# Kernel optimization log

Hardware: AMD Instinct MI355X
Metric: run time of the kernel (lower is better)

The kernel has to match this reference:

```python
import jax, jax.numpy as jnp
import numpy as np

K, R, A, F, T = 100000, 5, 8, 32, 96
ROTATION_DELTA = 1


def setup_inputs() -> dict:
    key = jax.random.key(0)
    k1, k2, k3, k4, k5, k6, k7 = jax.random.split(key, 7)
    # barycentric coordinates: last dim packs (vertex_index, weight)
    idx = jax.random.randint(k1, (K, R, A, 3), 0, K)
    w = jax.random.uniform(k2, (K, R, A, 3), dtype=jnp.float32)
    w = w / jnp.sum(w, axis=-1, keepdims=True)
    bary_coordinates = jnp.stack([idx.astype(jnp.float32), w], axis=-1)  # (K,R,A,3,2)
    mesh_signal = jax.random.normal(k3, (K, F), dtype=jnp.float32)
    # kernel from define_kernel_values (abstract): fixed prior interpolation weights (R,A,R,A)
    kernel = jax.random.normal(k4, (R, A, R, A), dtype=jnp.float32) * 0.1
    template_neighbor_weights = jax.random.normal(k5, (T, R, A, F), dtype=jnp.float32) * 0.05
    template_self_weights = jax.random.normal(k6, (T, 1, F), dtype=jnp.float32) * 0.05
    bias = jax.random.normal(k7, (T,), dtype=jnp.float32) * 0.01
    return {
        "mesh_signal": mesh_signal,
        "bary_coordinates": bary_coordinates,
        "kernel": kernel,
        "template_neighbor_weights": template_neighbor_weights,
        "template_self_weights": template_self_weights,
        "bias": bias,
    }


def reference(mesh_signal, bary_coordinates, kernel, template_neighbor_weights,
              template_self_weights, bias):
    # --- signal retrieval: barycentric gather + interpolation ---
    idx = bary_coordinates[..., 0].astype(jnp.int32)          # (K,R,A,3)
    bw = bary_coordinates[..., 1]                              # (K,R,A,3)
    gathered = mesh_signal[idx]                                # (K,R,A,3,F)
    interp = jnp.sum(bw[..., None] * gathered, axis=-2)        # (K,R,A,F)
    # --- prior kernel fold (include_prior=True) ---
    interp = jnp.einsum('raxy,kxyf->kraf', kernel, interp)     # (K,R,A,F)
    # --- center contribution ---
    conv_center = jnp.einsum('tef,kf->ket', template_self_weights, mesh_signal)  # (K,1,T)
    # --- per-rotation template fold (torch.range is end-inclusive -> A//delta + 1 rotations) ---
    orientations = list(range(0, A + 1, ROTATION_DELTA))
    conv_neighbor = jnp.stack(
        [jnp.einsum('traf,kraf->kt', template_neighbor_weights,
                    jnp.roll(interp, o, axis=2)) + bias
         for o in orientations],
        axis=1)                                                # (K,O,T)
    return jax.nn.relu(conv_center + conv_neighbor)            # (K,O,T)
```

## Files before the change

kernel.cpp:

```cpp
#include <hip/hip_runtime.h>
#include <hip/hip_bf16.h>
#include <stdint.h>


typedef __attribute__((ext_vector_type(8))) short short8;
typedef __attribute__((ext_vector_type(4))) float floatx4;
typedef __attribute__((ext_vector_type(2))) float fx2;

#define KPTS 100000
#define OUT_STRIDE 864
#define BM 64
#define THREADS 512
#define BP_SHORTS 1007616

#define BARRIER() do {                              \
    __builtin_amdgcn_sched_barrier(0);              \
    asm volatile("s_waitcnt lgkmcnt(0)");           \
    __builtin_amdgcn_s_barrier();                   \
  } while (0)

__device__ __forceinline__ short f2bf(float x) {
  union { float f; uint32_t u; } c; c.f = x;
  uint32_t u = c.u;
  u += 0x7FFFu + ((u >> 16) & 1u);
  return (short)(u >> 16);
}
__device__ __forceinline__ float bf2f(short s) {
  union { uint32_t u; float f; } c;
  c.u = ((uint32_t)(uint16_t)s) << 16;
  return c.f;
}

__global__ void prep_ms(const float* __restrict__ ms, short* __restrict__ msb) {
  const int i = (blockIdx.x * 256 + threadIdx.x) * 8;
  if (i < KPTS * 32) {
    floatx4 a = *(const floatx4*)(ms + i);
    floatx4 b = *(const floatx4*)(ms + i + 4);
    short8 s;
#pragma unroll
    for (int j = 0; j < 4; ++j) { s[j] = f2bf(a[j]); s[4 + j] = f2bf(b[j]); }
    *reinterpret_cast<short8*>(msb + i) = s;
  }
}

__global__ void prep_B(const float* __restrict__ kern,
                       const float* __restrict__ tw,
                       const float* __restrict__ sw,
                       short* __restrict__ Bp) {
  const int ntile = blockIdx.x;
  const int ch    = blockIdx.y;
  const int lane  = threadIdx.x;
  const int n = ntile * 16 + (lane & 15);
  const int o = n / 96;
  const int t = n - o * 96;
  const int fb = (lane >> 4) * 8;

  short8 v;
  if (ch < 40) {
    float kcol[40];
#pragma unroll
    for (int ra = 0; ra < 40; ++ra) kcol[ra] = kern[ra * 40 + ch];
#pragma unroll
    for (int j = 0; j < 8; ++j) {
      const int f = fb + j;
      float acc = 0.f;
      for (int r = 0; r < 5; ++r) {
#pragma unroll
        for (int a = 0; a < 8; ++a) {
          acc += kcol[r * 8 + a] * tw[((t * 5 + r) * 8 + ((a + o) & 7)) * 32 + f];
        }
      }
      v[j] = f2bf(acc);
    }
  } else {
#pragma unroll
    for (int j = 0; j < 8; ++j) v[j] = f2bf(sw[t * 32 + fb + j]);
  }
  *reinterpret_cast<short8*>(Bp + ((size_t)(ch * 48 + ntile) * 64 + lane) * 8) = v;
}

__global__ __launch_bounds__(THREADS, 1) void conv_main(
    const short* __restrict__ msb,
    const float* __restrict__ bary,
    const float* __restrict__ bias,
    const short* __restrict__ Bp,
    float* __restrict__ out) {
  __shared__ short Atile[2][BM][40];

  const int kbase = blockIdx.x * BM;
  const int tid = threadIdx.x;
  const int lane = tid & 63;
  const int wn = tid >> 6;
  const int l15 = lane & 15;
  const int kh = lane >> 4;

  const bool builder = tid < 256;
  const int arow = tid >> 2;
  const int af0 = (tid & 3) * 8;
  const int krow = kbase + (arow & 63);
  const bool rowok = builder && (krow < KPTS);
  const float* __restrict__ brow = bary + (size_t)(rowok ? krow : 0) * 240;
  const short* __restrict__ mrowb = msb + (size_t)(rowok ? krow : 0) * 32 + af0;

  fx2 bE0, bE1, bE2, bO0, bO1, bO2;
  short8 eG0, eG1, eG2, oG0, oG1, oG2;
  float eW0, eW1, eW2, oW0, oW1, oW2;

  auto ldbary = [&](int c, fx2& p0, fx2& p1, fx2& p2) {
    if (rowok) {
      const fx2* bp = (const fx2*)(brow + c * 6);
      p0 = __builtin_nontemporal_load(bp);
      p1 = __builtin_nontemporal_load(bp + 1);
      p2 = __builtin_nontemporal_load(bp + 2);
    } else {
      p0 = (fx2)0.f; p1 = (fx2)0.f; p2 = (fx2)0.f;
    }
  };
  auto issueG = [&](int c, const fx2& p0, const fx2& p1, const fx2& p2,
                    short8& A, short8& B, short8& C,
                    float& W0, float& W1, float& W2) {
    if (c == 40) {
      A = *(const short8*)(mrowb);
      B = A; C = A;
      W0 = rowok ? 1.f : 0.f; W1 = 0.f; W2 = 0.f;
    } else {
      A = *(const short8*)(msb + ((size_t)(int)p0.x) * 32 + af0);
      B = *(const short8*)(msb + ((size_t)(int)p1.x) * 32 + af0);
      C = *(const short8*)(msb + ((size_t)(int)p2.x) * 32 + af0);
      W0 = p0.y; W1 = p1.y; W2 = p2.y;
    }
  };
  auto commitG = [&](const short8& A, const short8& B, const short8& C,
                     float W0, float W1, float W2, int buf) {
    short8 s;
#pragma unroll
    for (int j = 0; j < 8; ++j)
      s[j] = f2bf(W0 * bf2f(A[j]) + W1 * bf2f(B[j]) + W2 * bf2f(C[j]));
    *reinterpret_cast<short8*>(&Atile[buf][arow][af0]) = s;
  };

  short8 bfA[6], bfB[6];
  auto loadB = [&](int c, short8* dst) {
    const short* bp = Bp + ((size_t)(c * 48 + wn * 6) * 64 + lane) * 8;
#pragma unroll
    for (int j = 0; j < 6; ++j)
      dst[j] = *reinterpret_cast<const short8*>(bp + (size_t)j * 512);
  };

  floatx4 acc[4][6];
#pragma unroll
  for (int mi = 0; mi < 4; ++mi)
#pragma unroll
    for (int nj = 0; nj < 6; ++nj) acc[mi][nj] = (floatx4)0.f;

  if (builder) {
    fx2 t0, t1, t2;
    ldbary(0, t0, t1, t2);
    issueG(0, t0, t1, t2, eG0, eG1, eG2, eW0, eW1, eW2);
    ldbary(1, t0, t1, t2);
    issueG(1, t0, t1, t2, oG0, oG1, oG2, oW0, oW1, oW2);
    ldbary(2, bE0, bE1, bE2);
    commitG(eG0, eG1, eG2, eW0, eW1, eW2, 0);
  }
  loadB(0, bfA);
  BARRIER();

#define ITER(ch, UB0, UB1, UB2, FB0, FB1, FB2,                                  \
             FG0, FG1, FG2, FW0, FW1, FW2,                                      \
             CG0, CG1, CG2, CW0, CW1, CW2, CUR, BF, NBF)                        \
  {                                                                             \
    if (builder) {                                                              \
      if ((ch) + 2 <= 40)                                                       \
        issueG((ch) + 2, UB0, UB1, UB2, FG0, FG1, FG2, FW0, FW1, FW2);          \
      if ((ch) + 3 <= 39) ldbary((ch) + 3, FB0, FB1, FB2);                      \
    }                                                                           \
    short8 af[4];                                                               \
    _Pragma("unroll")                                                           \
    for (int mi = 0; mi < 4; ++mi)                                              \
      af[mi] = *reinterpret_cast<const short8*>(&Atile[CUR][mi * 16 + l15][kh * 8]); \
    if ((ch) + 1 <= 40) loadB((ch) + 1, NBF);                                   \
    _Pragma("unroll")                                                           \
    for (int nj = 0; nj < 6; ++nj)                                              \
      _Pragma("unroll")                                                         \
      for (int mi = 0; mi < 4; ++mi)                                            \
        acc[mi][nj] = __builtin_amdgcn_mfma_f32_16x16x32_bf16(af[mi], BF[nj],   \
                                                              acc[mi][nj], 0, 0, 0); \
    if (builder && (ch) + 1 <= 40)                                              \
      commitG(CG0, CG1, CG2, CW0, CW1, CW2, (CUR) ^ 1);                         \
    BARRIER();                                                                  \
  }

  for (int ch = 0; ch < 40; ch += 2) {
    ITER(ch,     bE0, bE1, bE2, bO0, bO1, bO2,
         eG0, eG1, eG2, eW0, eW1, eW2,
         oG0, oG1, oG2, oW0, oW1, oW2, 0, bfA, bfB)
    ITER(ch + 1, bO0, bO1, bO2, bE0, bE1, bE2,
         oG0, oG1, oG2, oW0, oW1, oW2,
         eG0, eG1, eG2, eW0, eW1, eW2, 1, bfB, bfA)
  }
  ITER(40, bE0, bE1, bE2, bO0, bO1, bO2,
       eG0, eG1, eG2, eW0, eW1, eW2,
       oG0, oG1, oG2, oW0, oW1, oW2, 0, bfA, bfB)
#undef ITER

#pragma unroll
  for (int mi = 0; mi < 4; ++mi) {
    const int rb = kbase + mi * 16 + kh * 4;
#pragma unroll
    for (int nj = 0; nj < 6; ++nj) {
      const int n = wn * 96 + nj * 16 + l15;
      const float bsv = bias[nj * 16 + l15];
      const bool dup = (wn == 0);
#pragma unroll
      for (int i = 0; i < 4; ++i) {
        const int r = rb + i;
        if (r < KPTS) {
          float vv = fmaxf(acc[mi][nj][i] + bsv, 0.f);
          out[(size_t)r * OUT_STRIDE + n] = vv;
          if (dup) out[(size_t)r * OUT_STRIDE + 768 + n] = vv;
        }
      }
    }
  }
}

extern "C" void kernel_launch(void* const* d_in, const int* in_sizes, int n_in,
                              void* d_out, int out_size, void* d_ws, size_t ws_size,
                              hipStream_t stream) {
  const float* ms   = (const float*)d_in[0];
  const float* bary = (const float*)d_in[1];
  const float* kern = (const float*)d_in[2];
  const float* tw   = (const float*)d_in[3];
  const float* sw   = (const float*)d_in[4];
  const float* bias = (const float*)d_in[5];
  float* out = (float*)d_out;
  short* Bp  = (short*)d_ws;
  short* msb = (short*)d_ws + BP_SHORTS;

  hipLaunchKernelGGL(prep_B, dim3(48, 41), dim3(64), 0, stream, kern, tw, sw, Bp);
  hipLaunchKernelGGL(prep_ms, dim3((KPTS * 32 / 8 + 255) / 256), dim3(256), 0, stream,
                     ms, msb);
  hipLaunchKernelGGL(conv_main, dim3(1563), dim3(THREADS), 0, stream,
                     msb, bary, bias, Bp, out);
}
```

Before: 483.2 us.

## Warp-specialize conv kernel into gather-builder and MFMA-consumer waves

Raises the block to 1024 threads and splits the waves into roles. The first four waves only gather and interpolate mesh rows into the shared A tile. The remaining twelve waves only run bf16 MFMAs, each over four 16-column n-tiles instead of six. The aim is to overlap gather latency with matrix work and spread MFMA work over more waves. In exchange, the B fragments are no longer prefetched one chunk ahead, so their global-load latency sits right before the MFMAs. The launch bound asking for 4 blocks per CU also tightens the per-thread register budget, which may force spills.

```diff
diff --git a/kernel.cpp b/kernel.cpp
--- a/kernel.cpp
+++ b/kernel.cpp
@@ -10,7 +10,7 @@
 #define KPTS 100000
 #define OUT_STRIDE 864
 #define BM 64
-#define THREADS 512
+#define THREADS 1024
 #define BP_SHORTS 1007616
 
 #define BARRIER() do {                              \
@@ -79,7 +79,7 @@
   *reinterpret_cast<short8*>(Bp + ((size_t)(ch * 48 + ntile) * 64 + lane) * 8) = v;
 }
 
-__global__ __launch_bounds__(THREADS, 1) void conv_main(
+__global__ __launch_bounds__(THREADS, 4) void conv_main(
     const short* __restrict__ msb,
     const float* __restrict__ bary,
     const float* __restrict__ bias,
@@ -90,11 +90,13 @@
   const int kbase = blockIdx.x * BM;
   const int tid = threadIdx.x;
   const int lane = tid & 63;
-  const int wn = tid >> 6;
   const int l15 = lane & 15;
   const int kh = lane >> 4;
 
   const bool builder = tid < 256;
+  const bool consumer = tid >= 256;
+  const int wng = (tid >> 6) - 4;
+
   const int arow = tid >> 2;
   const int af0 = (tid & 3) * 8;
   const int krow = kbase + (arow & 63);
@@ -139,19 +141,19 @@
     *reinterpret_cast<short8*>(&Atile[buf][arow][af0]) = s;
   };
 
-  short8 bfA[6], bfB[6];
-  auto loadB = [&](int c, short8* dst) {
-    const short* bp = Bp + ((size_t)(c * 48 + wn * 6) * 64 + lane) * 8;
-#pragma unroll
-    for (int j = 0; j < 6; ++j)
-      dst[j] = *reinterpret_cast<const short8*>(bp + (size_t)j * 512);
-  };
-
-  floatx4 acc[4][6];
+  short8 bf[4];
+  auto loadB = [&](int c) {
+    const short* bp = Bp + ((size_t)(c * 48 + wng * 4) * 64 + lane) * 8;
+#pragma unroll
+    for (int j = 0; j < 4; ++j)
+      bf[j] = *reinterpret_cast<const short8*>(bp + (size_t)j * 512);
+  };
+
+  floatx4 acc[4][4];
 #pragma unroll
   for (int mi = 0; mi < 4; ++mi)
 #pragma unroll
-    for (int nj = 0; nj < 6; ++nj) acc[mi][nj] = (floatx4)0.f;
+    for (int nj = 0; nj < 4; ++nj) acc[mi][nj] = (floatx4)0.f;
 
   if (builder) {
     fx2 t0, t1, t2;
@@ -162,29 +164,30 @@
     ldbary(2, bE0, bE1, bE2);
     commitG(eG0, eG1, eG2, eW0, eW1, eW2, 0);
   }
-  loadB(0, bfA);
   BARRIER();
 
 #define ITER(ch, UB0, UB1, UB2, FB0, FB1, FB2,                                  \
              FG0, FG1, FG2, FW0, FW1, FW2,                                      \
-             CG0, CG1, CG2, CW0, CW1, CW2, CUR, BF, NBF)                        \
+             CG0, CG1, CG2, CW0, CW1, CW2, CUR)                                 \
   {                                                                             \
     if (builder) {                                                              \
       if ((ch) + 2 <= 40)                                                       \
         issueG((ch) + 2, UB0, UB1, UB2, FG0, FG1, FG2, FW0, FW1, FW2);          \
       if ((ch) + 3 <= 39) ldbary((ch) + 3, FB0, FB1, FB2);                      \
     }                                                                           \
-    short8 af[4];                                                               \
-    _Pragma("unroll")                                                           \
-    for (int mi = 0; mi < 4; ++mi)                                              \
-      af[mi] = *reinterpret_cast<const short8*>(&Atile[CUR][mi * 16 + l15][kh * 8]); \
-    if ((ch) + 1 <= 40) loadB((ch) + 1, NBF);                                   \
-    _Pragma("unroll")                                                           \
-    for (int nj = 0; nj < 6; ++nj)                                              \
+    if (consumer) {                                                             \
+      loadB(ch);                                                                \
+      short8 af[4];                                                             \
       _Pragma("unroll")                                                         \
       for (int mi = 0; mi < 4; ++mi)                                            \
-        acc[mi][nj] = __builtin_amdgcn_mfma_f32_16x16x32_bf16(af[mi], BF[nj],   \
-                                                              acc[mi][nj], 0, 0, 0); \
+        af[mi] = *reinterpret_cast<const short8*>(&Atile[CUR][mi * 16 + l15][kh * 8]); \
+      _Pragma("unroll")                                                         \
+      for (int nj = 0; nj < 4; ++nj)                                            \
+        _Pragma("unroll")                                                       \
+        for (int mi = 0; mi < 4; ++mi)                                          \
+          acc[mi][nj] = __builtin_amdgcn_mfma_f32_16x16x32_bf16(af[mi], bf[nj], \
+                                                                acc[mi][nj], 0, 0, 0); \
+    }                                                                           \
     if (builder && (ch) + 1 <= 40)                                              \
       commitG(CG0, CG1, CG2, CW0, CW1, CW2, (CUR) ^ 1);                         \
     BARRIER();                                                                  \
@@ -193,31 +196,33 @@
   for (int ch = 0; ch < 40; ch += 2) {
     ITER(ch,     bE0, bE1, bE2, bO0, bO1, bO2,
          eG0, eG1, eG2, eW0, eW1, eW2,
-         oG0, oG1, oG2, oW0, oW1, oW2, 0, bfA, bfB)
+         oG0, oG1, oG2, oW0, oW1, oW2, 0)
     ITER(ch + 1, bO0, bO1, bO2, bE0, bE1, bE2,
          oG0, oG1, oG2, oW0, oW1, oW2,
-         eG0, eG1, eG2, eW0, eW1, eW2, 1, bfB, bfA)
+         eG0, eG1, eG2, eW0, eW1, eW2, 1)
   }
   ITER(40, bE0, bE1, bE2, bO0, bO1, bO2,
        eG0, eG1, eG2, eW0, eW1, eW2,
-       oG0, oG1, oG2, oW0, oW1, oW2, 0, bfA, bfB)
+       oG0, oG1, oG2, oW0, oW1, oW2, 0)
 #undef ITER
 
-#pragma unroll
-  for (int mi = 0; mi < 4; ++mi) {
-    const int rb = kbase + mi * 16 + kh * 4;
-#pragma unroll
-    for (int nj = 0; nj < 6; ++nj) {
-      const int n = wn * 96 + nj * 16 + l15;
-      const float bsv = bias[nj * 16 + l15];
-      const bool dup = (wn == 0);
-#pragma unroll
-      for (int i = 0; i < 4; ++i) {
-        const int r = rb + i;
-        if (r < KPTS) {
-          float vv = fmaxf(acc[mi][nj][i] + bsv, 0.f);
-          out[(size_t)r * OUT_STRIDE + n] = vv;
-          if (dup) out[(size_t)r * OUT_STRIDE + 768 + n] = vv;
+  if (consumer) {
+#pragma unroll
+    for (int mi = 0; mi < 4; ++mi) {
+      const int rb = kbase + mi * 16 + kh * 4;
+#pragma unroll
+      for (int nj = 0; nj < 4; ++nj) {
+        const int n = wng * 64 + nj * 16 + l15;
+        const float bsv = bias[(wng * 64 + nj * 16) % 96 + l15];
+        const bool dup = (n < 96);
+#pragma unroll
+        for (int i = 0; i < 4; ++i) {
+          const int r = rb + i;
+          if (r < KPTS) {
+            float vv = fmaxf(acc[mi][nj][i] + bsv, 0.f);
+            out[(size_t)r * OUT_STRIDE + n] = vv;
+            if (dup) out[(size_t)r * OUT_STRIDE + 768 + n] = vv;
+          }
         }
       }
     }
```

Measured after the change: 1.179 ms. 2.44x slower.
